# Kernel optimization log

Measured on AMD Instinct MI355X. Metric: run time of the kernel, lower is better.

## Reference

```python
import jax, jax.numpy as jnp
import numpy as np

NUM_USERS = 200000
NUM_ARTISTS = 50000
LATENT_DIM = 64
NUM_EDGES = 2000000
NUM_LAYERS = 3


def setup_inputs() -> dict:
    key = jax.random.key(0)
    k_u, k_a, k_src, k_dst = jax.random.split(key, 4)
    x_users = jax.random.normal(k_u, (NUM_USERS, LATENT_DIM), dtype=jnp.float32)
    x_artists = jax.random.normal(k_a, (NUM_ARTISTS, LATENT_DIM), dtype=jnp.float32)
    # a2u: row 0 = artist (source) ids, row 1 = user (target) ids
    art = jax.random.randint(k_src, (NUM_EDGES,), 0, NUM_ARTISTS, dtype=jnp.int32)
    usr = jax.random.randint(k_dst, (NUM_EDGES,), 0, NUM_USERS, dtype=jnp.int32)
    edge_index_a2u = jnp.stack([art, usr], axis=0)
    # u2a is the reversed edge list: row 0 = user (source), row 1 = artist (target)
    edge_index_u2a = jnp.stack([usr, art], axis=0)
    return {
        "x_users": x_users,
        "x_artists": x_artists,
        "edge_index_a2u": edge_index_a2u,
        "edge_index_u2a": edge_index_u2a,
    }


def _scatter_mean(src_nodes, edge_index, dim_size):
    """Gather src_nodes[edge_index[0]] and scatter-mean onto edge_index[1].

    Matches torch_scatter.scatter(reduce='mean'): empty segments yield 0.
    """
    msgs = src_nodes[edge_index[0]]                     # [E, D] gather
    sums = jax.ops.segment_sum(msgs, edge_index[1], num_segments=dim_size)
    ones = jnp.ones((edge_index.shape[1],), dtype=src_nodes.dtype)
    counts = jax.ops.segment_sum(ones, edge_index[1], num_segments=dim_size)
    return sums / jnp.maximum(counts, 1.0)[:, None]


def reference(x_users, x_artists, edge_index_a2u, edge_index_u2a):
    scale = 1.0 / (NUM_LAYERS + 1)
    final_u = x_users * scale
    final_a = x_artists * scale
    for _ in range(NUM_LAYERS):
        x_users = _scatter_mean(x_artists, edge_index_a2u, NUM_USERS)
        x_artists = _scatter_mean(x_users, edge_index_u2a, NUM_ARTISTS)
        final_u = final_u + x_users * scale
        final_a = final_a + x_artists * scale
    return final_u, final_a
```

## Files before the change

kernel.cpp:

```cpp
#include <hip/hip_runtime.h>
#include <hip/hip_fp16.h>

#define D 64
#define TB 256

#define BSHIFT_U 10
#define BSHIFT_A 8
#define CAP   12288
#define CAP_P 16384
#define SENT  0xFFFFFFFFu

typedef _Float16 half8 __attribute__((ext_vector_type(8)));
typedef float float8 __attribute__((ext_vector_type(8)));

__device__ __forceinline__ float8 h8_to_f8(half8 h) {
    return __builtin_convertvector(h, float8);
}

__global__ __launch_bounds__(TB) void zero_ints_kernel(int* __restrict__ p, int n) {
    int i = blockIdx.x * blockDim.x + threadIdx.x;
    int stride = gridDim.x * blockDim.x;
    for (; i < n; i += stride) p[i] = 0;
}

__global__ __launch_bounds__(TB) void cvt_f16_kernel(const float4* __restrict__ in,
                                                     half8* __restrict__ out, int n8) {
    int i = blockIdx.x * blockDim.x + threadIdx.x;
    int stride = gridDim.x * blockDim.x;
    for (; i < n8; i += stride) {
        float4 a = in[i * 2 + 0];
        float4 b = in[i * 2 + 1];
        half8 h;
        h[0] = (_Float16)a.x; h[1] = (_Float16)a.y; h[2] = (_Float16)a.z; h[3] = (_Float16)a.w;
        h[4] = (_Float16)b.x; h[5] = (_Float16)b.y; h[6] = (_Float16)b.z; h[7] = (_Float16)b.w;
        out[i] = h;
    }
}

__global__ __launch_bounds__(TB) void partition_both_kernel(const int* __restrict__ art,
                                                            const int* __restrict__ usr, int E,
                                                            int* __restrict__ bcur_u,
                                                            int* __restrict__ bcur_a,
                                                            unsigned* __restrict__ part_u,
                                                            unsigned* __restrict__ part_a,
                                                            int NBu, int NBa) {
    __shared__ int cu[256], bu[256], ca[256], ba[256];
    for (int i = threadIdx.x; i < NBu; i += TB) cu[i] = 0;
    for (int i = threadIdx.x; i < NBa; i += TB) ca[i] = 0;
    __syncthreads();
    int chunk = (E + gridDim.x - 1) / gridDim.x;
    int e0 = blockIdx.x * chunk;
    int e1 = min(E, e0 + chunk);
    for (int e = e0 + threadIdx.x; e < e1; e += TB) {
        atomicAdd(&cu[usr[e] >> BSHIFT_U], 1);
        atomicAdd(&ca[art[e] >> BSHIFT_A], 1);
    }
    __syncthreads();
    for (int i = threadIdx.x; i < NBu; i += TB) {
        int c = cu[i];
        bu[i] = c ? (i * CAP_P + atomicAdd(&bcur_u[i], (c + 15) & ~15)) : 0;
        cu[i] = 0;
    }
    for (int i = threadIdx.x; i < NBa; i += TB) {
        int c = ca[i];
        ba[i] = c ? (i * CAP_P + atomicAdd(&bcur_a[i], (c + 15) & ~15)) : 0;
        ca[i] = 0;
    }
    __syncthreads();
    for (int e = e0 + threadIdx.x; e < e1; e += TB) {
        int a = art[e];
        int u = usr[e];
        int bui = u >> BSHIFT_U;
        int lu = atomicAdd(&cu[bui], 1);
        part_u[bu[bui] + lu] = ((unsigned)a << BSHIFT_U) | ((unsigned)u & ((1u << BSHIFT_U) - 1u));
        int bai = a >> BSHIFT_A;
        int la = atomicAdd(&ca[bai], 1);
        part_a[ba[bai] + la] = ((unsigned)u << BSHIFT_A) | ((unsigned)a & ((1u << BSHIFT_A) - 1u));
    }
    __syncthreads();
    for (int i = threadIdx.x; i < NBu; i += TB) {
        int c = cu[i];
        if (c) {
            int pad = (c + 15) & ~15;
            for (int k = c; k < pad; ++k) part_u[bu[i] + k] = SENT;
        }
    }
    for (int i = threadIdx.x; i < NBa; i += TB) {
        int c = ca[i];
        if (c) {
            int pad = (c + 15) & ~15;
            for (int k = c; k < pad; ++k) part_a[ba[i] + k] = SENT;
        }
    }
}

__device__ __forceinline__ void local_csr_body(const unsigned* __restrict__ part,
                                               int ecount, int ebeg_p, int ebeg_c, int n0,
                                               int2* __restrict__ rowdeg,
                                               int* __restrict__ csr,
                                               int N, int NPB, int BSHIFT,
                                               int* cnt, int* sdata) {
    const int tid = threadIdx.x;
    const int eend = ebeg_p + ecount;
    const unsigned mask = (unsigned)(NPB - 1);
    for (int i = tid; i < NPB; i += TB) cnt[i] = 0;
    __syncthreads();
    for (int e = ebeg_p + tid; e < eend; e += TB) {
        unsigned r = part[e];
        if (r != SENT) atomicAdd(&cnt[r & mask], 1);
    }
    __syncthreads();
    const int ITEMS = NPB >> 8;
    const int ib = tid * ITEMS;
    int local = 0;
    for (int k = 0; k < ITEMS; ++k) local += cnt[ib + k];
    sdata[tid] = local;
    __syncthreads();
    for (int off = 1; off < TB; off <<= 1) {
        int t = (tid >= off) ? sdata[tid - off] : 0;
        __syncthreads();
        if (tid >= off) sdata[tid] += t;
        __syncthreads();
    }
    int run = sdata[tid] - local;
    for (int k = 0; k < ITEMS; ++k) {
        int v = cnt[ib + k];
        cnt[ib + k] = run;
        int n = n0 + ib + k;
        if (n < N) rowdeg[n] = make_int2(ebeg_c + run, v);
        run += v;
    }
    __syncthreads();
    for (int e = ebeg_p + tid; e < eend; e += TB) {
        unsigned r = part[e];
        if (r == SENT) continue;
        int l = (int)(r & mask);
        int pos = atomicAdd(&cnt[l], 1);
        csr[ebeg_c + pos] = (int)(r >> BSHIFT);
    }
}

__global__ __launch_bounds__(TB) void local_csr_both_kernel(const unsigned* __restrict__ part_u,
                                                            const unsigned* __restrict__ part_a,
                                                            const int* __restrict__ bcur_u,
                                                            const int* __restrict__ bcur_a,
                                                            int2* __restrict__ rowdeg_u,
                                                            int2* __restrict__ rowdeg_a,
                                                            int* __restrict__ csr_u,
                                                            int* __restrict__ csr_a,
                                                            int NU, int NA, int NBu) {
    __shared__ int cnt[1024];
    __shared__ int sdata[TB];
    const int b = blockIdx.x;
    if (b < NBu) {
        local_csr_body(part_u, bcur_u[b], b * CAP_P, b * CAP, b << BSHIFT_U,
                       rowdeg_u, csr_u, NU, 1 << BSHIFT_U, BSHIFT_U, cnt, sdata);
    } else {
        const int bb = b - NBu;
        local_csr_body(part_a, bcur_a[bb], bb * CAP_P, bb * CAP, bb << BSHIFT_A,
                       rowdeg_a, csr_a, NA, 1 << BSHIFT_A, BSHIFT_A, cnt, sdata);
    }
}

__global__ __launch_bounds__(TB) void gather_mean_kernel(const half8* __restrict__ src,
                                                         const int* __restrict__ csr,
                                                         const int2* __restrict__ rowdeg,
                                                         half8* __restrict__ x_out,
                                                         float4* __restrict__ final_acc,
                                                         const float4* __restrict__ init_src,
                                                         const float4* __restrict__ fin_in0,
                                                         const half8* __restrict__ fin_x1,
                                                         const half8* __restrict__ fin_x2,
                                                         float4* __restrict__ fin_out,
                                                         int N, float scale) {
    const int lane = threadIdx.x & 7;
    int g = (blockIdx.x * blockDim.x + threadIdx.x) >> 3;
    const int ngroups = (gridDim.x * blockDim.x) >> 3;
    for (int n = g; n < N; n += ngroups) {
        const int2 rd = rowdeg[n];
        const int beg = rd.x;
        const int dg = rd.y;
        const int end = beg + dg;
        float8 a0 = 0.f, a1 = 0.f, a2 = 0.f, a3 = 0.f;
        int e = beg;
        for (; e + 4 <= end; e += 4) {
            const int s0 = csr[e + 0];
            const int s1 = csr[e + 1];
            const int s2 = csr[e + 2];
            const int s3 = csr[e + 3];
            const half8 v0 = src[s0 * 8 + lane];
            const half8 v1 = src[s1 * 8 + lane];
            const half8 v2 = src[s2 * 8 + lane];
            const half8 v3 = src[s3 * 8 + lane];
            a0 += h8_to_f8(v0);
            a1 += h8_to_f8(v1);
            a2 += h8_to_f8(v2);
            a3 += h8_to_f8(v3);
        }
        for (; e < end; ++e)
            a0 += h8_to_f8(src[csr[e] * 8 + lane]);
        float8 s = (a0 + a1) + (a2 + a3);
        const float inv = 1.f / (float)(dg > 0 ? dg : 1);
        float8 x = s * inv;
        const int o8 = n * 8 + lane;
        if (x_out != nullptr) {
            half8 h;
            for (int k = 0; k < 8; ++k) h[k] = (_Float16)x[k];
            x_out[o8] = h;
        }
        const int fo = n * (D / 4) + lane * 2;
        if (fin_out != nullptr) {
            float8 t = h8_to_f8(fin_x1[o8]) + h8_to_f8(fin_x2[o8]) + x;
            float4 f0 = fin_in0[fo + 0];
            float4 f1 = fin_in0[fo + 1];
            f0.x = (f0.x + t[0]) * scale; f0.y = (f0.y + t[1]) * scale;
            f0.z = (f0.z + t[2]) * scale; f0.w = (f0.w + t[3]) * scale;
            f1.x = (f1.x + t[4]) * scale; f1.y = (f1.y + t[5]) * scale;
            f1.z = (f1.z + t[6]) * scale; f1.w = (f1.w + t[7]) * scale;
            fin_out[fo + 0] = f0;
            fin_out[fo + 1] = f1;
        }
        if (final_acc != nullptr) {
            float4 f0, f1;
            if (init_src != nullptr) {
                f0 = init_src[fo + 0];
                f1 = init_src[fo + 1];
                f0.x *= scale; f0.y *= scale; f0.z *= scale; f0.w *= scale;
                f1.x *= scale; f1.y *= scale; f1.z *= scale; f1.w *= scale;
            } else {
                f0 = final_acc[fo + 0];
                f1 = final_acc[fo + 1];
            }
            f0.x += x[0] * scale; f0.y += x[1] * scale; f0.z += x[2] * scale; f0.w += x[3] * scale;
            f1.x += x[4] * scale; f1.y += x[5] * scale; f1.z += x[6] * scale; f1.w += x[7] * scale;
            final_acc[fo + 0] = f0;
            final_acc[fo + 1] = f1;
        }
    }
}

extern "C" void kernel_launch(void* const* d_in, const int* in_sizes, int n_in,
                              void* d_out, int out_size, void* d_ws, size_t ws_size,
                              hipStream_t stream) {
    const float* x_users   = (const float*)d_in[0];
    const float* x_artists = (const float*)d_in[1];
    const int*   a2u       = (const int*)d_in[2];

    const int NU = in_sizes[0] / D;
    const int NA = in_sizes[1] / D;
    const int E  = in_sizes[2] / 2;
    const int* art = a2u;
    const int* usr = a2u + E;

    const float scale = 0.25f;

    const int NBu = (NU + (1 << BSHIFT_U) - 1) >> BSHIFT_U;
    const int NBa = (NA + (1 << BSHIFT_A) - 1) >> BSHIFT_A;

    char* w = (char*)d_ws;
    size_t off = 0;
    auto alloc = [&](size_t bytes) -> char* {
        char* p = w + off;
        off += (bytes + 255) & ~(size_t)255;
        return p;
    };
    int2* rowdeg_u = (int2*)alloc((size_t)NU * 8);
    int2* rowdeg_a = (int2*)alloc((size_t)NA * 8);
    int* bcur      = (int*)alloc((size_t)(NBu + NBa) * 4);
    int* bcur_u    = bcur;
    int* bcur_a    = bcur + NBu;
    int* csr_u     = (int*)alloc((size_t)NBu * CAP * 4);
    int* csr_a     = (int*)alloc((size_t)NBa * CAP * 4);
    half8* xa_in   = (half8*)alloc((size_t)NA * D * 2);
    unsigned* part_u = (unsigned*)alloc((size_t)NBu * CAP_P * 4);
    unsigned* part_a = (unsigned*)alloc((size_t)NBa * CAP_P * 4);

    const size_t XU = (size_t)NU * D * 2;
    const size_t XA = (size_t)NA * D * 2;
    const size_t XUa = (XU + 255) & ~(size_t)255;
    const size_t XAa = (XA + 255) & ~(size_t)255;

    const bool modeA = (off + 3 * XUa) <= ws_size;

    half8* x_u1 = (half8*)alloc(XU);
    half8* x_u2 = modeA ? (half8*)alloc(XU) : x_u1;
    half8* x_u3 = modeA ? (half8*)alloc(XU) : x_u1;
    char* part_base = (char*)part_u;
    half8* x_a1 = (half8*)(part_base);
    half8* x_a2 = modeA ? (half8*)(part_base + XAa) : x_a1;
    half8* x_a3 = modeA ? (half8*)(part_base + 2 * XAa) : x_a1;

    float* out_u = (float*)d_out;
    float* out_a = out_u + (size_t)NU * D;

    cvt_f16_kernel<<<1024, TB, 0, stream>>>((const float4*)x_artists, xa_in, NA * D / 8);
    zero_ints_kernel<<<1, TB, 0, stream>>>(bcur, NBu + NBa);
    partition_both_kernel<<<256, TB, 0, stream>>>(art, usr, E, bcur_u, bcur_a,
                                                  part_u, part_a, NBu, NBa);
    local_csr_both_kernel<<<NBu + NBa, TB, 0, stream>>>(part_u, part_a, bcur_u, bcur_a,
                                                        rowdeg_u, rowdeg_a,
                                                        csr_u, csr_a, NU, NA, NBu);

    half8* xu_buf[3] = {x_u1, x_u2, x_u3};
    half8* xa_buf[3] = {x_a1, x_a2, x_a3};
    const half8* srcA = xa_in;
    for (int l = 0; l < 3; ++l) {
        const bool last = (l == 2);
        gather_mean_kernel<<<4096, TB, 0, stream>>>(
            srcA, csr_u, rowdeg_u, xu_buf[l],
            modeA ? nullptr : (float4*)out_u,
            (!modeA && l == 0) ? (const float4*)x_users : nullptr,
            (modeA && last) ? (const float4*)x_users : nullptr,
            (modeA && last) ? x_u1 : nullptr,
            (modeA && last) ? x_u2 : nullptr,
            (modeA && last) ? (float4*)out_u : nullptr,
            NU, scale);
        gather_mean_kernel<<<4096, TB, 0, stream>>>(
            xu_buf[l], csr_a, rowdeg_a,
            (modeA && last) ? nullptr : xa_buf[l],
            modeA ? nullptr : (float4*)out_a,
            (!modeA && l == 0) ? (const float4*)x_artists : nullptr,
            (modeA && last) ? (const float4*)x_artists : nullptr,
            (modeA && last) ? x_a1 : nullptr,
            (modeA && last) ? x_a2 : nullptr,
            (modeA && last) ? (float4*)out_a : nullptr,
            NA, scale);
        srcA = xa_buf[l];
    }
}
```

Baseline: 376.5 us.

## Split artist features into halves and gather users in two cache-resident passes

Artist fp16 features are stored as two 32-dim halves in separate planes. The user gather now runs in two passes, each reading only one half-plane, so the randomly accessed source table is small enough to stay in each XCD's L2. The cost is reading the CSR index stream twice per layer. Separately, CSR, rowdeg and streaming output accesses use nontemporal loads and stores, and the zero-init and fp16 convert kernels are fused into one launch.

```diff
diff --git a/kernel.cpp b/kernel.cpp
--- a/kernel.cpp
+++ b/kernel.cpp
@@ -12,28 +12,31 @@
 
 typedef _Float16 half8 __attribute__((ext_vector_type(8)));
 typedef float float8 __attribute__((ext_vector_type(8)));
+typedef float f32x4 __attribute__((ext_vector_type(4)));
 
 __device__ __forceinline__ float8 h8_to_f8(half8 h) {
     return __builtin_convertvector(h, float8);
 }
-
-__global__ __launch_bounds__(TB) void zero_ints_kernel(int* __restrict__ p, int n) {
+template <typename T>
+__device__ __forceinline__ T ntl(const T* p) { return __builtin_nontemporal_load(p); }
+template <typename T>
+__device__ __forceinline__ void nts(T* p, T v) { __builtin_nontemporal_store(v, p); }
+
+__global__ __launch_bounds__(TB) void cvt_split_zero_kernel(const f32x4* __restrict__ in,
+                                                            half8* __restrict__ out, int NA,
+                                                            int* __restrict__ bcur, int nb) {
     int i = blockIdx.x * blockDim.x + threadIdx.x;
     int stride = gridDim.x * blockDim.x;
-    for (; i < n; i += stride) p[i] = 0;
-}
-
-__global__ __launch_bounds__(TB) void cvt_f16_kernel(const float4* __restrict__ in,
-                                                     half8* __restrict__ out, int n8) {
-    int i = blockIdx.x * blockDim.x + threadIdx.x;
-    int stride = gridDim.x * blockDim.x;
-    for (; i < n8; i += stride) {
-        float4 a = in[i * 2 + 0];
-        float4 b = in[i * 2 + 1];
+    for (int j = i; j < nb; j += stride) bcur[j] = 0;
+    int n8 = NA * 8;
+    for (int j = i; j < n8; j += stride) {
+        int a = j >> 3, k = j & 7;
+        f32x4 x0 = in[a * 16 + k * 2];
+        f32x4 x1 = in[a * 16 + k * 2 + 1];
         half8 h;
-        h[0] = (_Float16)a.x; h[1] = (_Float16)a.y; h[2] = (_Float16)a.z; h[3] = (_Float16)a.w;
-        h[4] = (_Float16)b.x; h[5] = (_Float16)b.y; h[6] = (_Float16)b.z; h[7] = (_Float16)b.w;
-        out[i] = h;
+        h[0] = (_Float16)x0[0]; h[1] = (_Float16)x0[1]; h[2] = (_Float16)x0[2]; h[3] = (_Float16)x0[3];
+        h[4] = (_Float16)x1[0]; h[5] = (_Float16)x1[1]; h[6] = (_Float16)x1[2]; h[7] = (_Float16)x1[3];
+        out[(size_t)(k >> 2) * (NA * 4) + a * 4 + (k & 3)] = h;
     }
 }
 
@@ -162,79 +165,140 @@
     }
 }
 
-__global__ __launch_bounds__(TB) void gather_mean_kernel(const half8* __restrict__ src,
+__global__ __launch_bounds__(TB) void gather_user_kernel(const half8* __restrict__ srcp,
                                                          const int* __restrict__ csr,
                                                          const int2* __restrict__ rowdeg,
                                                          half8* __restrict__ x_out,
-                                                         float4* __restrict__ final_acc,
-                                                         const float4* __restrict__ init_src,
-                                                         const float4* __restrict__ fin_in0,
+                                                         const f32x4* __restrict__ fin_in0,
                                                          const half8* __restrict__ fin_x1,
                                                          const half8* __restrict__ fin_x2,
-                                                         float4* __restrict__ fin_out,
-                                                         int N, float scale) {
+                                                         f32x4* __restrict__ fin_out,
+                                                         f32x4* __restrict__ final_acc,
+                                                         const f32x4* __restrict__ init_src,
+                                                         int N, int p, float scale) {
+    const int lane = threadIdx.x & 3;
+    int g = (blockIdx.x * blockDim.x + threadIdx.x) >> 2;
+    const int ngroups = (gridDim.x * blockDim.x) >> 2;
+    for (int n = g; n < N; n += ngroups) {
+        const long long rdl = ntl((const long long*)&rowdeg[n]);
+        const int beg = (int)(unsigned)(rdl & 0xFFFFFFFFll);
+        const int dg  = (int)(rdl >> 32);
+        const int end = beg + dg;
+        float8 a0 = 0.f, a1 = 0.f, a2 = 0.f, a3 = 0.f;
+        int e = beg;
+        for (; e + 4 <= end; e += 4) {
+            const int s0 = ntl(&csr[e + 0]);
+            const int s1 = ntl(&csr[e + 1]);
+            const int s2 = ntl(&csr[e + 2]);
+            const int s3 = ntl(&csr[e + 3]);
+            a0 += h8_to_f8(srcp[s0 * 4 + lane]);
+            a1 += h8_to_f8(srcp[s1 * 4 + lane]);
+            a2 += h8_to_f8(srcp[s2 * 4 + lane]);
+            a3 += h8_to_f8(srcp[s3 * 4 + lane]);
+        }
+        for (; e < end; ++e)
+            a0 += h8_to_f8(srcp[ntl(&csr[e]) * 4 + lane]);
+        float8 s = (a0 + a1) + (a2 + a3);
+        const float inv = 1.f / (float)(dg > 0 ? dg : 1);
+        float8 x = s * inv;
+        const int xo = n * 8 + p * 4 + lane;
+        if (x_out != nullptr) {
+            half8 h;
+            for (int k = 0; k < 8; ++k) h[k] = (_Float16)x[k];
+            nts(&x_out[xo], h);
+        }
+        const int fo = n * 16 + p * 8 + lane * 2;
+        if (fin_out != nullptr) {
+            float8 t = h8_to_f8(ntl(&fin_x1[xo])) + h8_to_f8(ntl(&fin_x2[xo])) + x;
+            f32x4 f0 = ntl(&fin_in0[fo + 0]);
+            f32x4 f1 = ntl(&fin_in0[fo + 1]);
+            f32x4 t0 = {t[0], t[1], t[2], t[3]};
+            f32x4 t1 = {t[4], t[5], t[6], t[7]};
+            nts(&fin_out[fo + 0], (f0 + t0) * scale);
+            nts(&fin_out[fo + 1], (f1 + t1) * scale);
+        }
+        if (final_acc != nullptr) {
+            f32x4 f0, f1;
+            if (init_src != nullptr) {
+                f0 = ntl(&init_src[fo + 0]) * scale;
+                f1 = ntl(&init_src[fo + 1]) * scale;
+            } else {
+                f0 = final_acc[fo + 0];
+                f1 = final_acc[fo + 1];
+            }
+            f32x4 x0 = {x[0], x[1], x[2], x[3]};
+            f32x4 x1 = {x[4], x[5], x[6], x[7]};
+            final_acc[fo + 0] = f0 + x0 * scale;
+            final_acc[fo + 1] = f1 + x1 * scale;
+        }
+    }
+}
+
+__global__ __launch_bounds__(TB) void gather_artist_kernel(const half8* __restrict__ src,
+                                                           const int* __restrict__ csr,
+                                                           const int2* __restrict__ rowdeg,
+                                                           half8* __restrict__ x_out_split,
+                                                           const f32x4* __restrict__ fin_in0,
+                                                           const half8* __restrict__ fin_x1,
+                                                           const half8* __restrict__ fin_x2,
+                                                           f32x4* __restrict__ fin_out,
+                                                           f32x4* __restrict__ final_acc,
+                                                           const f32x4* __restrict__ init_src,
+                                                           int N, int split_stride, float scale) {
     const int lane = threadIdx.x & 7;
     int g = (blockIdx.x * blockDim.x + threadIdx.x) >> 3;
     const int ngroups = (gridDim.x * blockDim.x) >> 3;
     for (int n = g; n < N; n += ngroups) {
-        const int2 rd = rowdeg[n];
-        const int beg = rd.x;
-        const int dg = rd.y;
+        const long long rdl = ntl((const long long*)&rowdeg[n]);
+        const int beg = (int)(unsigned)(rdl & 0xFFFFFFFFll);
+        const int dg  = (int)(rdl >> 32);
         const int end = beg + dg;
         float8 a0 = 0.f, a1 = 0.f, a2 = 0.f, a3 = 0.f;
         int e = beg;
         for (; e + 4 <= end; e += 4) {
-            const int s0 = csr[e + 0];
-            const int s1 = csr[e + 1];
-            const int s2 = csr[e + 2];
-            const int s3 = csr[e + 3];
-            const half8 v0 = src[s0 * 8 + lane];
-            const half8 v1 = src[s1 * 8 + lane];
-            const half8 v2 = src[s2 * 8 + lane];
-            const half8 v3 = src[s3 * 8 + lane];
-            a0 += h8_to_f8(v0);
-            a1 += h8_to_f8(v1);
-            a2 += h8_to_f8(v2);
-            a3 += h8_to_f8(v3);
+            const int s0 = ntl(&csr[e + 0]);
+            const int s1 = ntl(&csr[e + 1]);
+            const int s2 = ntl(&csr[e + 2]);
+            const int s3 = ntl(&csr[e + 3]);
+            a0 += h8_to_f8(src[s0 * 8 + lane]);
+            a1 += h8_to_f8(src[s1 * 8 + lane]);
+            a2 += h8_to_f8(src[s2 * 8 + lane]);
+            a3 += h8_to_f8(src[s3 * 8 + lane]);
         }
         for (; e < end; ++e)
-            a0 += h8_to_f8(src[csr[e] * 8 + lane]);
+            a0 += h8_to_f8(src[ntl(&csr[e]) * 8 + lane]);
         float8 s = (a0 + a1) + (a2 + a3);
         const float inv = 1.f / (float)(dg > 0 ? dg : 1);
         float8 x = s * inv;
-        const int o8 = n * 8 + lane;
-        if (x_out != nullptr) {
+        const int sidx = (lane >> 2) * split_stride + n * 4 + (lane & 3);
+        if (x_out_split != nullptr) {
             half8 h;
             for (int k = 0; k < 8; ++k) h[k] = (_Float16)x[k];
-            x_out[o8] = h;
-        }
-        const int fo = n * (D / 4) + lane * 2;
+            nts(&x_out_split[sidx], h);
+        }
+        const int fo = n * 16 + lane * 2;
         if (fin_out != nullptr) {
-            float8 t = h8_to_f8(fin_x1[o8]) + h8_to_f8(fin_x2[o8]) + x;
-            float4 f0 = fin_in0[fo + 0];
-            float4 f1 = fin_in0[fo + 1];
-            f0.x = (f0.x + t[0]) * scale; f0.y = (f0.y + t[1]) * scale;
-            f0.z = (f0.z + t[2]) * scale; f0.w = (f0.w + t[3]) * scale;
-            f1.x = (f1.x + t[4]) * scale; f1.y = (f1.y + t[5]) * scale;
-            f1.z = (f1.z + t[6]) * scale; f1.w = (f1.w + t[7]) * scale;
-            fin_out[fo + 0] = f0;
-            fin_out[fo + 1] = f1;
+            float8 t = h8_to_f8(ntl(&fin_x1[sidx])) + h8_to_f8(ntl(&fin_x2[sidx])) + x;
+            f32x4 f0 = ntl(&fin_in0[fo + 0]);
+            f32x4 f1 = ntl(&fin_in0[fo + 1]);
+            f32x4 t0 = {t[0], t[1], t[2], t[3]};
+            f32x4 t1 = {t[4], t[5], t[6], t[7]};
+            nts(&fin_out[fo + 0], (f0 + t0) * scale);
+            nts(&fin_out[fo + 1], (f1 + t1) * scale);
         }
         if (final_acc != nullptr) {
-            float4 f0, f1;
+            f32x4 f0, f1;
             if (init_src != nullptr) {
-                f0 = init_src[fo + 0];
-                f1 = init_src[fo + 1];
-                f0.x *= scale; f0.y *= scale; f0.z *= scale; f0.w *= scale;
-                f1.x *= scale; f1.y *= scale; f1.z *= scale; f1.w *= scale;
+                f0 = ntl(&init_src[fo + 0]) * scale;
+                f1 = ntl(&init_src[fo + 1]) * scale;
             } else {
                 f0 = final_acc[fo + 0];
                 f1 = final_acc[fo + 1];
             }
-            f0.x += x[0] * scale; f0.y += x[1] * scale; f0.z += x[2] * scale; f0.w += x[3] * scale;
-            f1.x += x[4] * scale; f1.y += x[5] * scale; f1.z += x[6] * scale; f1.w += x[7] * scale;
-            final_acc[fo + 0] = f0;
-            final_acc[fo + 1] = f1;
+            f32x4 x0 = {x[0], x[1], x[2], x[3]};
+            f32x4 x1 = {x[4], x[5], x[6], x[7]};
+            final_acc[fo + 0] = f0 + x0 * scale;
+            final_acc[fo + 1] = f1 + x1 * scale;
         }
     }
 }
@@ -256,6 +320,7 @@
 
     const int NBu = (NU + (1 << BSHIFT_U) - 1) >> BSHIFT_U;
     const int NBa = (NA + (1 << BSHIFT_A) - 1) >> BSHIFT_A;
+    const int SPLIT_STRIDE = NA * 4;
 
     char* w = (char*)d_ws;
     size_t off = 0;
@@ -288,13 +353,12 @@
     char* part_base = (char*)part_u;
     half8* x_a1 = (half8*)(part_base);
     half8* x_a2 = modeA ? (half8*)(part_base + XAa) : x_a1;
-    half8* x_a3 = modeA ? (half8*)(part_base + 2 * XAa) : x_a1;
 
     float* out_u = (float*)d_out;
     float* out_a = out_u + (size_t)NU * D;
 
-    cvt_f16_kernel<<<1024, TB, 0, stream>>>((const float4*)x_artists, xa_in, NA * D / 8);
-    zero_ints_kernel<<<1, TB, 0, stream>>>(bcur, NBu + NBa);
+    cvt_split_zero_kernel<<<1024, TB, 0, stream>>>((const f32x4*)x_artists, xa_in, NA,
+                                                   bcur, NBu + NBa);
     partition_both_kernel<<<256, TB, 0, stream>>>(art, usr, E, bcur_u, bcur_a,
                                                   part_u, part_a, NBu, NBa);
     local_csr_both_kernel<<<NBu + NBa, TB, 0, stream>>>(part_u, part_a, bcur_u, bcur_a,
@@ -302,29 +366,32 @@
                                                         csr_u, csr_a, NU, NA, NBu);
 
     half8* xu_buf[3] = {x_u1, x_u2, x_u3};
-    half8* xa_buf[3] = {x_a1, x_a2, x_a3};
+    half8* xa_buf[3] = {x_a1, x_a2, nullptr};
     const half8* srcA = xa_in;
     for (int l = 0; l < 3; ++l) {
         const bool last = (l == 2);
-        gather_mean_kernel<<<4096, TB, 0, stream>>>(
-            srcA, csr_u, rowdeg_u, xu_buf[l],
-            modeA ? nullptr : (float4*)out_u,
-            (!modeA && l == 0) ? (const float4*)x_users : nullptr,
-            (modeA && last) ? (const float4*)x_users : nullptr,
-            (modeA && last) ? x_u1 : nullptr,
-            (modeA && last) ? x_u2 : nullptr,
-            (modeA && last) ? (float4*)out_u : nullptr,
-            NU, scale);
-        gather_mean_kernel<<<4096, TB, 0, stream>>>(
+        for (int p = 0; p < 2; ++p) {
+            gather_user_kernel<<<4096, TB, 0, stream>>>(
+                srcA + (size_t)p * SPLIT_STRIDE, csr_u, rowdeg_u, xu_buf[l],
+                (modeA && last) ? (const f32x4*)x_users : nullptr,
+                (modeA && last) ? x_u1 : nullptr,
+                (modeA && last) ? x_u2 : nullptr,
+                (modeA && last) ? (f32x4*)out_u : nullptr,
+                modeA ? nullptr : (f32x4*)out_u,
+                (!modeA && l == 0) ? (const f32x4*)x_users : nullptr,
+                NU, p, scale);
+        }
+        gather_artist_kernel<<<2048, TB, 0, stream>>>(
             xu_buf[l], csr_a, rowdeg_a,
-            (modeA && last) ? nullptr : xa_buf[l],
-            modeA ? nullptr : (float4*)out_a,
-            (!modeA && l == 0) ? (const float4*)x_artists : nullptr,
-            (modeA && last) ? (const float4*)x_artists : nullptr,
+            (modeA && last) ? nullptr : xa_buf[modeA ? l : 0],
+            (modeA && last) ? (const f32x4*)x_artists : nullptr,
             (modeA && last) ? x_a1 : nullptr,
             (modeA && last) ? x_a2 : nullptr,
-            (modeA && last) ? (float4*)out_a : nullptr,
-            NA, scale);
-        srcA = xa_buf[l];
-    }
-}
+            (modeA && last) ? (f32x4*)out_a : nullptr,
+            modeA ? nullptr : (f32x4*)out_a,
+            (!modeA && l == 0) ? (const f32x4*)x_artists : nullptr,
+            NA, SPLIT_STRIDE, scale);
+        srcA = modeA ? xa_buf[l] : xa_buf[0];
+        if (modeA && last) srcA = nullptr;
+    }
+}
```

Measured after the change: 460.5 us. +22.3%, slower.

## Sort CSR neighbours by source range, fuse zeroing, add nontemporal final writes

Applied to the files above, without the earlier changes.

The local CSR build now bins each row's edges by the high bits of the source index, so every row's neighbour list comes out coarsely sorted by source id. This should improve cache locality of the gathers across the three layers. The counter-zeroing kernel is merged into the fp16 conversion kernel, which removes one launch. The final accumulation uses nontemporal loads and stores, and the artist gather launches half as many blocks. The cost is larger shared histograms (4096 ints) and a longer scan in the CSR build.

```diff
diff --git a/kernel.cpp b/kernel.cpp
--- a/kernel.cpp
+++ b/kernel.cpp
@@ -9,31 +9,33 @@
 #define CAP   12288
 #define CAP_P 16384
 #define SENT  0xFFFFFFFFu
+#define TSHIFT 14
 
 typedef _Float16 half8 __attribute__((ext_vector_type(8)));
 typedef float float8 __attribute__((ext_vector_type(8)));
+typedef float f32x4 __attribute__((ext_vector_type(4)));
 
 __device__ __forceinline__ float8 h8_to_f8(half8 h) {
     return __builtin_convertvector(h, float8);
 }
-
-__global__ __launch_bounds__(TB) void zero_ints_kernel(int* __restrict__ p, int n) {
+template <typename T>
+__device__ __forceinline__ T ntl(const T* p) { return __builtin_nontemporal_load(p); }
+template <typename T>
+__device__ __forceinline__ void nts(T* p, T v) { __builtin_nontemporal_store(v, p); }
+
+__global__ __launch_bounds__(TB) void cvt_f16_zero_kernel(const f32x4* __restrict__ in,
+                                                          half8* __restrict__ out, int n8,
+                                                          int* __restrict__ bcur, int nb) {
     int i = blockIdx.x * blockDim.x + threadIdx.x;
     int stride = gridDim.x * blockDim.x;
-    for (; i < n; i += stride) p[i] = 0;
-}
-
-__global__ __launch_bounds__(TB) void cvt_f16_kernel(const float4* __restrict__ in,
-                                                     half8* __restrict__ out, int n8) {
-    int i = blockIdx.x * blockDim.x + threadIdx.x;
-    int stride = gridDim.x * blockDim.x;
-    for (; i < n8; i += stride) {
-        float4 a = in[i * 2 + 0];
-        float4 b = in[i * 2 + 1];
+    for (int j = i; j < nb; j += stride) bcur[j] = 0;
+    for (int j = i; j < n8; j += stride) {
+        f32x4 a = in[j * 2 + 0];
+        f32x4 b = in[j * 2 + 1];
         half8 h;
-        h[0] = (_Float16)a.x; h[1] = (_Float16)a.y; h[2] = (_Float16)a.z; h[3] = (_Float16)a.w;
-        h[4] = (_Float16)b.x; h[5] = (_Float16)b.y; h[6] = (_Float16)b.z; h[7] = (_Float16)b.w;
-        out[i] = h;
+        h[0] = (_Float16)a[0]; h[1] = (_Float16)a[1]; h[2] = (_Float16)a[2]; h[3] = (_Float16)a[3];
+        h[4] = (_Float16)b[0]; h[5] = (_Float16)b[1]; h[6] = (_Float16)b[2]; h[7] = (_Float16)b[3];
+        out[j] = h;
     }
 }
 
@@ -94,23 +96,27 @@
     }
 }
 
+template <int NPB, int NB, int BSHIFT>
 __device__ __forceinline__ void local_csr_body(const unsigned* __restrict__ part,
                                                int ecount, int ebeg_p, int ebeg_c, int n0,
                                                int2* __restrict__ rowdeg,
-                                               int* __restrict__ csr,
-                                               int N, int NPB, int BSHIFT,
+                                               int* __restrict__ csr, int N,
                                                int* cnt, int* sdata) {
     const int tid = threadIdx.x;
+    const int NBINS = NPB * NB;
     const int eend = ebeg_p + ecount;
     const unsigned mask = (unsigned)(NPB - 1);
-    for (int i = tid; i < NPB; i += TB) cnt[i] = 0;
+    for (int i = tid; i < NBINS; i += TB) cnt[i] = 0;
     __syncthreads();
     for (int e = ebeg_p + tid; e < eend; e += TB) {
         unsigned r = part[e];
-        if (r != SENT) atomicAdd(&cnt[r & mask], 1);
-    }
-    __syncthreads();
-    const int ITEMS = NPB >> 8;
+        if (r != SENT) {
+            int bin = (int)(r & mask) * NB + (int)((r >> BSHIFT) >> TSHIFT);
+            atomicAdd(&cnt[bin], 1);
+        }
+    }
+    __syncthreads();
+    const int ITEMS = NBINS / TB;
     const int ib = tid * ITEMS;
     int local = 0;
     for (int k = 0; k < ITEMS; ++k) local += cnt[ib + k];
@@ -123,19 +129,26 @@
         __syncthreads();
     }
     int run = sdata[tid] - local;
-    for (int k = 0; k < ITEMS; ++k) {
-        int v = cnt[ib + k];
-        cnt[ib + k] = run;
-        int n = n0 + ib + k;
-        if (n < N) rowdeg[n] = make_int2(ebeg_c + run, v);
-        run += v;
+    const int NPT = ITEMS / NB;
+    for (int j = 0; j < NPT; ++j) {
+        const int nodeStart = run;
+        int d = 0;
+        for (int k = 0; k < NB; ++k) {
+            int idx = ib + j * NB + k;
+            int v = cnt[idx];
+            cnt[idx] = run;
+            run += v;
+            d += v;
+        }
+        int n = n0 + (ib / NB) + j;
+        if (n < N) rowdeg[n] = make_int2(ebeg_c + nodeStart, d);
     }
     __syncthreads();
     for (int e = ebeg_p + tid; e < eend; e += TB) {
         unsigned r = part[e];
         if (r == SENT) continue;
-        int l = (int)(r & mask);
-        int pos = atomicAdd(&cnt[l], 1);
+        int bin = (int)(r & mask) * NB + (int)((r >> BSHIFT) >> TSHIFT);
+        int pos = atomicAdd(&cnt[bin], 1);
         csr[ebeg_c + pos] = (int)(r >> BSHIFT);
     }
 }
@@ -149,16 +162,16 @@
                                                             int* __restrict__ csr_u,
                                                             int* __restrict__ csr_a,
                                                             int NU, int NA, int NBu) {
-    __shared__ int cnt[1024];
+    __shared__ int cnt[4096];
     __shared__ int sdata[TB];
     const int b = blockIdx.x;
     if (b < NBu) {
-        local_csr_body(part_u, bcur_u[b], b * CAP_P, b * CAP, b << BSHIFT_U,
-                       rowdeg_u, csr_u, NU, 1 << BSHIFT_U, BSHIFT_U, cnt, sdata);
+        local_csr_body<1024, 4, BSHIFT_U>(part_u, bcur_u[b], b * CAP_P, b * CAP,
+                                          b << BSHIFT_U, rowdeg_u, csr_u, NU, cnt, sdata);
     } else {
         const int bb = b - NBu;
-        local_csr_body(part_a, bcur_a[bb], bb * CAP_P, bb * CAP, bb << BSHIFT_A,
-                       rowdeg_a, csr_a, NA, 1 << BSHIFT_A, BSHIFT_A, cnt, sdata);
+        local_csr_body<256, 16, BSHIFT_A>(part_a, bcur_a[bb], bb * CAP_P, bb * CAP,
+                                          bb << BSHIFT_A, rowdeg_a, csr_a, NA, cnt, sdata);
     }
 }
 
@@ -166,12 +179,12 @@
                                                          const int* __restrict__ csr,
                                                          const int2* __restrict__ rowdeg,
                                                          half8* __restrict__ x_out,
-                                                         float4* __restrict__ final_acc,
-                                                         const float4* __restrict__ init_src,
-                                                         const float4* __restrict__ fin_in0,
+                                                         f32x4* __restrict__ final_acc,
+                                                         const f32x4* __restrict__ init_src,
+                                                         const f32x4* __restrict__ fin_in0,
                                                          const half8* __restrict__ fin_x1,
                                                          const half8* __restrict__ fin_x2,
-                                                         float4* __restrict__ fin_out,
+                                                         f32x4* __restrict__ fin_out,
                                                          int N, float scale) {
     const int lane = threadIdx.x & 7;
     int g = (blockIdx.x * blockDim.x + threadIdx.x) >> 3;
@@ -188,14 +201,10 @@
             const int s1 = csr[e + 1];
             const int s2 = csr[e + 2];
             const int s3 = csr[e + 3];
-            const half8 v0 = src[s0 * 8 + lane];
-            const half8 v1 = src[s1 * 8 + lane];
-            const half8 v2 = src[s2 * 8 + lane];
-            const half8 v3 = src[s3 * 8 + lane];
-            a0 += h8_to_f8(v0);
-            a1 += h8_to_f8(v1);
-            a2 += h8_to_f8(v2);
-            a3 += h8_to_f8(v3);
+            a0 += h8_to_f8(src[s0 * 8 + lane]);
+            a1 += h8_to_f8(src[s1 * 8 + lane]);
+            a2 += h8_to_f8(src[s2 * 8 + lane]);
+            a3 += h8_to_f8(src[s3 * 8 + lane]);
         }
         for (; e < end; ++e)
             a0 += h8_to_f8(src[csr[e] * 8 + lane]);
@@ -210,31 +219,27 @@
         }
         const int fo = n * (D / 4) + lane * 2;
         if (fin_out != nullptr) {
-            float8 t = h8_to_f8(fin_x1[o8]) + h8_to_f8(fin_x2[o8]) + x;
-            float4 f0 = fin_in0[fo + 0];
-            float4 f1 = fin_in0[fo + 1];
-            f0.x = (f0.x + t[0]) * scale; f0.y = (f0.y + t[1]) * scale;
-            f0.z = (f0.z + t[2]) * scale; f0.w = (f0.w + t[3]) * scale;
-            f1.x = (f1.x + t[4]) * scale; f1.y = (f1.y + t[5]) * scale;
-            f1.z = (f1.z + t[6]) * scale; f1.w = (f1.w + t[7]) * scale;
-            fin_out[fo + 0] = f0;
-            fin_out[fo + 1] = f1;
+            float8 t = h8_to_f8(ntl(&fin_x1[o8])) + h8_to_f8(ntl(&fin_x2[o8])) + x;
+            f32x4 f0 = ntl(&fin_in0[fo + 0]);
+            f32x4 f1 = ntl(&fin_in0[fo + 1]);
+            f32x4 t0 = {t[0], t[1], t[2], t[3]};
+            f32x4 t1 = {t[4], t[5], t[6], t[7]};
+            nts(&fin_out[fo + 0], (f0 + t0) * scale);
+            nts(&fin_out[fo + 1], (f1 + t1) * scale);
         }
         if (final_acc != nullptr) {
-            float4 f0, f1;
+            f32x4 f0, f1;
             if (init_src != nullptr) {
-                f0 = init_src[fo + 0];
-                f1 = init_src[fo + 1];
-                f0.x *= scale; f0.y *= scale; f0.z *= scale; f0.w *= scale;
-                f1.x *= scale; f1.y *= scale; f1.z *= scale; f1.w *= scale;
+                f0 = init_src[fo + 0] * scale;
+                f1 = init_src[fo + 1] * scale;
             } else {
                 f0 = final_acc[fo + 0];
                 f1 = final_acc[fo + 1];
             }
-            f0.x += x[0] * scale; f0.y += x[1] * scale; f0.z += x[2] * scale; f0.w += x[3] * scale;
-            f1.x += x[4] * scale; f1.y += x[5] * scale; f1.z += x[6] * scale; f1.w += x[7] * scale;
-            final_acc[fo + 0] = f0;
-            final_acc[fo + 1] = f1;
+            f32x4 x0 = {x[0], x[1], x[2], x[3]};
+            f32x4 x1 = {x[4], x[5], x[6], x[7]};
+            final_acc[fo + 0] = f0 + x0 * scale;
+            final_acc[fo + 1] = f1 + x1 * scale;
         }
     }
 }
@@ -288,13 +293,12 @@
     char* part_base = (char*)part_u;
     half8* x_a1 = (half8*)(part_base);
     half8* x_a2 = modeA ? (half8*)(part_base + XAa) : x_a1;
-    half8* x_a3 = modeA ? (half8*)(part_base + 2 * XAa) : x_a1;
 
     float* out_u = (float*)d_out;
     float* out_a = out_u + (size_t)NU * D;
 
-    cvt_f16_kernel<<<1024, TB, 0, stream>>>((const float4*)x_artists, xa_in, NA * D / 8);
-    zero_ints_kernel<<<1, TB, 0, stream>>>(bcur, NBu + NBa);
+    cvt_f16_zero_kernel<<<1024, TB, 0, stream>>>((const f32x4*)x_artists, xa_in,
+                                                 NA * D / 8, bcur, NBu + NBa);
     partition_both_kernel<<<256, TB, 0, stream>>>(art, usr, E, bcur_u, bcur_a,
                                                   part_u, part_a, NBu, NBa);
     local_csr_both_kernel<<<NBu + NBa, TB, 0, stream>>>(part_u, part_a, bcur_u, bcur_a,
@@ -302,29 +306,29 @@
                                                         csr_u, csr_a, NU, NA, NBu);
 
     half8* xu_buf[3] = {x_u1, x_u2, x_u3};
-    half8* xa_buf[3] = {x_a1, x_a2, x_a3};
+    half8* xa_buf[2] = {x_a1, x_a2};
     const half8* srcA = xa_in;
     for (int l = 0; l < 3; ++l) {
         const bool last = (l == 2);
         gather_mean_kernel<<<4096, TB, 0, stream>>>(
             srcA, csr_u, rowdeg_u, xu_buf[l],
-            modeA ? nullptr : (float4*)out_u,
-            (!modeA && l == 0) ? (const float4*)x_users : nullptr,
-            (modeA && last) ? (const float4*)x_users : nullptr,
+            modeA ? nullptr : (f32x4*)out_u,
+            (!modeA && l == 0) ? (const f32x4*)x_users : nullptr,
+            (modeA && last) ? (const f32x4*)x_users : nullptr,
             (modeA && last) ? x_u1 : nullptr,
             (modeA && last) ? x_u2 : nullptr,
-            (modeA && last) ? (float4*)out_u : nullptr,
+            (modeA && last) ? (f32x4*)out_u : nullptr,
             NU, scale);
-        gather_mean_kernel<<<4096, TB, 0, stream>>>(
+        gather_mean_kernel<<<2048, TB, 0, stream>>>(
             xu_buf[l], csr_a, rowdeg_a,
-            (modeA && last) ? nullptr : xa_buf[l],
-            modeA ? nullptr : (float4*)out_a,
-            (!modeA && l == 0) ? (const float4*)x_artists : nullptr,
-            (modeA && last) ? (const float4*)x_artists : nullptr,
+            (modeA && last) ? nullptr : (modeA ? xa_buf[l] : x_a1),
+            modeA ? nullptr : (f32x4*)out_a,
+            (!modeA && l == 0) ? (const f32x4*)x_artists : nullptr,
+            (modeA && last) ? (const f32x4*)x_artists : nullptr,
             (modeA && last) ? x_a1 : nullptr,
             (modeA && last) ? x_a2 : nullptr,
-            (modeA && last) ? (float4*)out_a : nullptr,
+            (modeA && last) ? (f32x4*)out_a : nullptr,
             NA, scale);
-        srcA = xa_buf[l];
-    }
-}
+        srcA = modeA ? xa_buf[l < 2 ? l : 0] : x_a1;
+    }
+}
```

Result: faster. 359.2 us (-4.6%).
